# Optimization experiments

Measured on AMD Instinct MI355X. Metric: run time of the kernel, lower is better.

The kernel has to match this reference:

```python
import jax, jax.numpy as jnp
import numpy as np

# static sizes (see shape_source)
OBJ_N, WALL_N, FLOOR_N = 192, 16, 1
T = OBJ_N + WALL_N + FLOOR_N          # 209 total nodes
R = T * T - T                          # 43472 directed edges (no self loops)
D = 512
STEPS = 4                              # feat_update_step (1 group)
OBJ_IN, WALL_IN, FLOOR_IN, REL_IN = 42, 15, 16, 2

# buildMap: all-pairs meshgrid edges, self-loops removed, one-hot subj/obj maps
_nd = ~np.eye(T, dtype=bool)
_si, _oi = np.meshgrid(np.arange(T), np.arange(T), indexing='ij')
_subj_idx = _si[_nd]
_obj_idx = _oi[_nd]
SUBJ_MAP = jnp.asarray((np.arange(T)[:, None] == _subj_idx[None, :]).astype(np.float32))  # [T,R]
OBJ_MAP = jnp.asarray((np.arange(T)[:, None] == _obj_idx[None, :]).astype(np.float32))    # [T,R]
TOTAL_MAP = jnp.ones((T, T), jnp.float32)
REL_IDX = jnp.asarray(np.nonzero(_nd.reshape(-1))[0])  # [R] static gather indices


def setup_inputs():
    key = jax.random.key(0)
    ks = iter(jax.random.split(key, 64))
    def w(shape):
        return jax.random.normal(next(ks), shape, jnp.float32) * 0.01  # normal_(0, 0.01)
    inp = {
        'cat_object_feature': jax.random.normal(next(ks), (1, OBJ_N, OBJ_IN), jnp.float32),
        'cat_wall_feature': jax.random.normal(next(ks), (1, WALL_N, WALL_IN), jnp.float32),
        'cat_floor_feature': jax.random.normal(next(ks), (1, FLOOR_N, FLOOR_IN), jnp.float32),
        'cat_relation_feature': jax.random.normal(next(ks), (1, OBJ_N * OBJ_N, REL_IN), jnp.float32),
    }
    for name, din in [('obj', OBJ_IN), ('wall', WALL_IN), ('floor', FLOOR_IN), ('rel', REL_IN)]:
        inp[name + '_w1'] = w((din, D)); inp[name + '_b1'] = jnp.zeros((D,), jnp.float32)
        inp[name + '_w2'] = w((D, D));   inp[name + '_b2'] = jnp.zeros((D,), jnp.float32)
    inp['collect_w'] = w((5, D, D))                       # 5 _Collection_Unit fc weights
    inp['collect_b'] = jnp.zeros((5, D), jnp.float32)
    for name in ['tr', 'eu', 'sc']:
        inp[name + '_w1'] = w((D, D // 2)); inp[name + '_b1'] = jnp.zeros((D // 2,), jnp.float32)
        inp[name + '_w2'] = w((D // 2, 3)); inp[name + '_b2'] = jnp.zeros((3,), jnp.float32)
    return inp


def _mlp(x, w1, b1, w2, b2):
    return jax.nn.relu(x @ w1 + b1) @ w2 + b2


def _head(x, w1, b1, w2, b2):
    # Linear -> LeakyReLU(0.2) -> Dropout(eval: identity) -> Linear
    return jax.nn.leaky_relu(x @ w1 + b1, 0.2) @ w2 + b2


def _collect(src, attn, w, b):
    # _Collection_Unit: attn @ relu(fc(src)) / (row_sum + 1e-7)
    fc = jax.nn.relu(src @ w + b)
    return (attn @ fc) / (attn.sum(1, keepdims=True) + 1e-7)


def reference(cat_object_feature, cat_wall_feature, cat_floor_feature, cat_relation_feature,
              obj_w1, obj_b1, obj_w2, obj_b2, wall_w1, wall_b1, wall_w2, wall_b2,
              floor_w1, floor_b1, floor_w2, floor_b2, rel_w1, rel_b1, rel_w2, rel_b2,
              collect_w, collect_b, tr_w1, tr_b1, tr_w2, tr_b2,
              eu_w1, eu_b1, eu_w2, eu_b2, sc_w1, sc_b1, sc_w2, sc_b2):
    tot = jnp.concatenate([
        _mlp(cat_object_feature[0], obj_w1, obj_b1, obj_w2, obj_b2),
        _mlp(cat_wall_feature[0], wall_w1, wall_b1, wall_w2, wall_b2),
        _mlp(cat_floor_feature[0], floor_w1, floor_b1, floor_w2, floor_b2)], axis=0)  # [T,D]
    emb_rel = _mlp(cat_relation_feature[0], rel_w1, rel_b1, rel_w2, rel_b2)
    padded = jnp.pad(emb_rel.reshape(OBJ_N, OBJ_N, D),
                     ((0, T - OBJ_N), (0, T - OBJ_N), (0, 0)), constant_values=0.001)
    rel = padded.reshape(T * T, D)[REL_IDX]  # mask_total_relation_feature [R,D]

    for _ in range(STEPS):
        s_obj = _collect(tot, TOTAL_MAP, collect_w[4], collect_b[4])
        s_rs = _collect(rel, SUBJ_MAP, collect_w[0], collect_b[0])
        s_ro = _collect(rel, OBJ_MAP, collect_w[1], collect_b[1])
        new_tot = tot + (s_obj + s_rs + s_ro) / 3.0          # _Update_Unit: target + source
        s_os = _collect(tot, SUBJ_MAP.T, collect_w[2], collect_b[2])
        s_oo = _collect(tot, OBJ_MAP.T, collect_w[3], collect_b[3])
        rel = rel + (s_os + s_oo) / 2.0
        tot = new_tot

    obj = tot[:OBJ_N]  # object_mask select
    return jnp.concatenate([
        _head(obj, tr_w1, tr_b1, tr_w2, tr_b2),
        _head(obj, eu_w1, eu_b1, eu_w2, eu_b2),
        _head(obj, sc_w1, sc_b1, sc_w2, sc_b2)], axis=-1)  # [OBJ_N, 9]
```

## Files before the change

### kernel.cpp

```cpp
#include <hip/hip_runtime.h>
#include <stdint.h>

typedef unsigned short u16;
typedef __attribute__((ext_vector_type(4))) float f32x4;
typedef __attribute__((ext_vector_type(8))) short s16x8;
typedef __attribute__((ext_vector_type(4))) short s16x4;

#define DD (512*512)

__device__ inline u16 f2bf(float f) {
  uint32_t u = __float_as_uint(f);
  u = (u + 0x7FFFu + ((u >> 16) & 1u)) >> 16;
  return (u16)u;
}
__device__ inline float bflo(uint32_t w) { return __uint_as_float(w << 16); }
__device__ inline float bfhi(uint32_t w) { return __uint_as_float(w & 0xFFFF0000u); }
__device__ inline f32x4 relu4(f32x4 v) {
  f32x4 r;
  r.x = fmaxf(v.x, 0.f); r.y = fmaxf(v.y, 0.f);
  r.z = fmaxf(v.z, 0.f); r.w = fmaxf(v.w, 0.f);
  return r;
}
__device__ inline f32x4 bf4(const u16* p) {
  uint2 w = *(const uint2*)p;
  f32x4 r; r.x = bflo(w.x); r.y = bfhi(w.x); r.z = bflo(w.y); r.w = bfhi(w.y);
  return r;
}
__device__ inline s16x4 pack4(f32x4 v) {
  s16x4 o;
  o[0] = (short)f2bf(v.x); o[1] = (short)f2bf(v.y);
  o[2] = (short)f2bf(v.z); o[3] = (short)f2bf(v.w);
  return o;
}
__device__ inline void gload16(const void* g, void* l) {
  __builtin_amdgcn_global_load_lds(
      (const __attribute__((address_space(1))) void*)g,
      (__attribute__((address_space(3))) void*)l, 16, 0, 0);
}

struct PrepP {
  const float *xo, *xw, *xf;
  const float *ow1, *ob1, *ww1, *wb1, *fw1, *fb1;
  float* hid;
  const float* rw2; u16* rw2b;
  const float* cw; u16* cwT;
  const float* cb; const float* rb2;
  float *b0b, *b0p, *b1b, *b1p;
  const float *xr, *rw1, *rb1; u16* Hh;
};

__global__ __launch_bounds__(256) void kprep(PrepP pp) {
  __shared__ __align__(16) float plds[1088];
  const int bid = blockIdx.x;
  const int t = threadIdx.x;
  if (bid < 209) {
    int tc = bid;
    const float* x; const float* w; const float* b; int K;
    if (tc < 192)      { x = pp.xo + tc * 42;         w = pp.ow1; b = pp.ob1; K = 42; }
    else if (tc < 208) { x = pp.xw + (tc - 192) * 15; w = pp.ww1; b = pp.wb1; K = 15; }
    else               { x = pp.xf;                   w = pp.fw1; b = pp.fb1; K = 16; }
    float* xs = plds;
    if (t < K) xs[t] = x[t];
    __syncthreads();
    #pragma unroll
    for (int dd = 0; dd < 2; dd++) {
      int d = t + dd * 256;
      float acc = b[d];
      for (int k = 0; k < K; k++) acc = fmaf(xs[k], w[k * 512 + d], acc);
      pp.hid[(size_t)tc * 512 + d] = fmaxf(acc, 0.f);
    }
  } else if (bid < 337) {
    int g = (bid - 209) * 256 + t;
    f32x4 a = *(const f32x4*)&pp.rw2[(size_t)g * 8];
    f32x4 b = *(const f32x4*)&pp.rw2[(size_t)g * 8 + 4];
    s16x8 o;
    o[0] = (short)f2bf(a.x); o[1] = (short)f2bf(a.y); o[2] = (short)f2bf(a.z); o[3] = (short)f2bf(a.w);
    o[4] = (short)f2bf(b.x); o[5] = (short)f2bf(b.y); o[6] = (short)f2bf(b.z); o[7] = (short)f2bf(b.w);
    *(s16x8*)&pp.rw2b[(size_t)g * 8] = o;
  } else if (bid < 1617) {
    int local = bid - 337;
    int bx = local & 15, by = (local >> 4) & 15, bz = local >> 8;
    float (*tile)[33] = (float(*)[33])plds;
    const float* src = pp.cw + (size_t)bz * DD;
    int k0 = bx * 32, n0 = by * 32;
    #pragma unroll
    for (int i = 0; i < 4; i++) {
      int idx = t + i * 256; int r = idx >> 5, c = idx & 31;
      tile[r][c] = src[(size_t)(k0 + r) * 512 + n0 + c];
    }
    __syncthreads();
    #pragma unroll
    for (int i = 0; i < 4; i++) {
      int idx = t + i * 256; int r = idx >> 5, c = idx & 31;
      pp.cwT[((size_t)bz * 512 + n0 + r) * 512 + k0 + c] = f2bf(tile[c][r]);
    }
  } else if (bid < 1625) {
    int bx = bid - 1617;
    int dl = t & 63;
    int d = bx * 64 + dl;
    int kg = t >> 6;
    const float* W0 = pp.cw;
    const float* W1 = pp.cw + DD;
    float a0 = 0, p0 = 0, a1 = 0, p1 = 0;
    for (int k = kg * 128; k < (kg + 1) * 128; ++k) {
      float w0 = W0[(size_t)k * 512 + d], w1 = W1[(size_t)k * 512 + d], r = pp.rb2[k];
      a0 = fmaf(r, w0, a0); p0 += w0;
      a1 = fmaf(r, w1, a1); p1 += w1;
    }
    float (*red)[4][64] = (float(*)[4][64])plds;
    red[0][kg][dl] = a0; red[1][kg][dl] = p0; red[2][kg][dl] = a1; red[3][kg][dl] = p1;
    __syncthreads();
    if (kg == 0) {
      float s0  = red[0][0][dl] + red[0][1][dl] + red[0][2][dl] + red[0][3][dl];
      float sp0 = red[1][0][dl] + red[1][1][dl] + red[1][2][dl] + red[1][3][dl];
      float s1  = red[2][0][dl] + red[2][1][dl] + red[2][2][dl] + red[2][3][dl];
      float sp1 = red[3][0][dl] + red[3][1][dl] + red[3][2][dl] + red[3][3][dl];
      float bb0 = pp.cb[0 * 512 + d], bb1 = pp.cb[1 * 512 + d];
      pp.b0b[d] = s0 + bb0;
      pp.b0p[d] = 0.001f * sp0 + bb0;
      pp.b1b[d] = s1 + bb1;
      pp.b1p[d] = 0.001f * sp1 + bb1;
    }
  } else {
    int gid = (bid - 1625) * 256 + t;
    int m = gid >> 6;
    int dg = (gid & 63) * 8;
    float x0 = pp.xr[m * 2], x1 = pp.xr[m * 2 + 1];
    s16x8 o;
    #pragma unroll
    for (int j = 0; j < 8; j++) {
      int dd = dg + j;
      float v = fmaf(x0, pp.rw1[dd], fmaf(x1, pp.rw1[512 + dd], pp.rb1[dd]));
      o[j] = (short)f2bf(fmaxf(v, 0.f));
    }
    *(s16x8*)&pp.Hh[(size_t)m * 512 + dg] = o;
  }
}

struct SJob { const float* A; const float* B; const float* bias; float* C; u16* Cb; int M; int act; };
struct SJobs { SJob j[4]; int cum[5]; int njobs; };
struct PMJob { const u16* A; const u16* BT; float* C; };
struct MidP { SJobs sj; PMJob mj[2]; };

__global__ __launch_bounds__(256) void kmid(MidP mp) {
  __shared__ __align__(16) u16 mlds[24576];
  const int t = threadIdx.x;
  if (blockIdx.x < 64) {
    int bi = blockIdx.x;
    int ji = 0;
    while (ji + 1 < mp.sj.njobs && bi >= mp.sj.cum[ji + 1]) ji++;
    SJob job = mp.sj.j[ji];
    int local = bi - mp.sj.cum[ji];
    int mt = local >> 3, nt = local & 7;
    int m0 = mt * 32, n0 = nt * 64;
    float* As = (float*)mlds;
    float* Bs = As + 32 * 36;
    int row = t >> 3;
    int cg  = (t & 7) * 8;
    f32x4 accA = {0.f,0.f,0.f,0.f}, accB = {0.f,0.f,0.f,0.f};
    for (int k0 = 0; k0 < 512; k0 += 32) {
      __syncthreads();
      {
        int ar = t >> 3, ac = (t & 7) * 4;
        f32x4 av = {0.f,0.f,0.f,0.f};
        if (m0 + ar < job.M) av = *(const f32x4*)&job.A[(size_t)(m0 + ar) * 512 + k0 + ac];
        *(f32x4*)&As[ar * 36 + ac] = av;
      }
      #pragma unroll
      for (int i = 0; i < 2; i++) {
        int idx = t + i * 256;
        int bk = idx >> 4, bn = (idx & 15) * 4;
        *(f32x4*)&Bs[bk * 64 + bn] = *(const f32x4*)&job.B[(size_t)(k0 + bk) * 512 + n0 + bn];
      }
      __syncthreads();
      #pragma unroll
      for (int kk = 0; kk < 32; kk += 4) {
        f32x4 a4 = *(const f32x4*)&As[row * 36 + kk];
        #pragma unroll
        for (int q = 0; q < 4; q++) {
          f32x4 b0 = *(const f32x4*)&Bs[(kk + q) * 64 + cg];
          f32x4 b1 = *(const f32x4*)&Bs[(kk + q) * 64 + cg + 4];
          float av = a4[q];
          accA += av * b0;
          accB += av * b1;
        }
      }
    }
    int r = m0 + row;
    if (r < job.M) {
      f32x4 b0 = {0.f,0.f,0.f,0.f}, b1 = {0.f,0.f,0.f,0.f};
      if (job.bias) { b0 = *(const f32x4*)&job.bias[n0 + cg]; b1 = *(const f32x4*)&job.bias[n0 + cg + 4]; }
      f32x4 o0 = accA + b0, o1 = accB + b1;
      if (job.act) { o0 = relu4(o0); o1 = relu4(o1); }
      *(f32x4*)&job.C[(size_t)r * 512 + n0 + cg]     = o0;
      *(f32x4*)&job.C[(size_t)r * 512 + n0 + cg + 4] = o1;
      if (job.Cb) {
        s16x8 ob;
        ob[0] = (short)f2bf(o0.x); ob[1] = (short)f2bf(o0.y);
        ob[2] = (short)f2bf(o0.z); ob[3] = (short)f2bf(o0.w);
        ob[4] = (short)f2bf(o1.x); ob[5] = (short)f2bf(o1.y);
        ob[6] = (short)f2bf(o1.z); ob[7] = (short)f2bf(o1.w);
        *(s16x8*)&job.Cb[(size_t)r * 512 + n0 + cg] = ob;
      }
    }
  } else {
    int bi = blockIdx.x - 64;
    int ji = bi >> 5;
    int local = bi & 31;
    PMJob job = mp.mj[ji];
    int m0 = (local >> 2) * 64, n0 = (local & 3) * 128;
    u16* smem = mlds;
    const int lane = t & 63;
    const int wave = t >> 6;
    const int wm = wave >> 1, wn = wave & 1;
    const int r16 = lane & 15;
    const int kq = lane >> 4;
    f32x4 acc[2][4];
    #pragma unroll
    for (int i = 0; i < 2; i++)
      #pragma unroll
      for (int j = 0; j < 4; j++) acc[i][j] = (f32x4){0.f,0.f,0.f,0.f};
    const u16* gA[2]; int laofs[2];
    const u16* gB[4]; int lbofs[4];
    #pragma unroll
    for (int i = 0; i < 2; i++) {
      int seg = i * 256 + t;
      int row = seg >> 3, s = seg & 7;
      gA[i] = job.A + (size_t)(m0 + row) * 512 + ((s ^ (row & 7)) << 3);
      laofs[i] = (i * 256 + (t & 192)) << 3;
    }
    #pragma unroll
    for (int i = 0; i < 4; i++) {
      int seg = i * 256 + t;
      int row = seg >> 3, s = seg & 7;
      gB[i] = job.BT + (size_t)(n0 + row) * 512 + ((s ^ (row & 7)) << 3);
      lbofs[i] = 4096 + ((i * 256 + (t & 192)) << 3);
    }
    #pragma unroll
    for (int i = 0; i < 2; i++) gload16(gA[i], smem + laofs[i]);
    #pragma unroll
    for (int i = 0; i < 4; i++) gload16(gB[i], smem + lbofs[i]);
    __syncthreads();
    int buf = 0;
    for (int it = 0; it < 8; ++it) {
      if (it < 7) {
        int nb = (buf ^ 1) * 12288;
        int k0n = (it + 1) * 64;
        #pragma unroll
        for (int i = 0; i < 2; i++) gload16(gA[i] + k0n, smem + nb + laofs[i]);
        #pragma unroll
        for (int i = 0; i < 4; i++) gload16(gB[i] + k0n, smem + nb + lbofs[i]);
      }
      const u16* Ab = smem + buf * 12288;
      const u16* Bb = Ab + 4096;
      #pragma unroll
      for (int kh = 0; kh < 2; kh++) {
        s16x8 af[2], bfr[4];
        #pragma unroll
        for (int i = 0; i < 2; i++) {
          int r = wm * 32 + i * 16 + r16;
          af[i] = *(const s16x8*)&Ab[r * 64 + (((kq + kh * 4) ^ (r & 7)) << 3)];
        }
        #pragma unroll
        for (int j = 0; j < 4; j++) {
          int r = wn * 64 + j * 16 + r16;
          bfr[j] = *(const s16x8*)&Bb[r * 64 + (((kq + kh * 4) ^ (r & 7)) << 3)];
        }
        #pragma unroll
        for (int i = 0; i < 2; i++)
          #pragma unroll
          for (int j = 0; j < 4; j++)
            acc[i][j] = __builtin_amdgcn_mfma_f32_16x16x32_bf16(af[i], bfr[j], acc[i][j], 0, 0, 0);
      }
      __syncthreads();
      buf ^= 1;
    }
    #pragma unroll
    for (int i = 0; i < 2; i++) {
      int rbase = m0 + wm * 32 + i * 16 + (lane >> 4) * 4;
      #pragma unroll
      for (int r = 0; r < 4; r++) {
        int grow = rbase + r;
        #pragma unroll
        for (int j = 0; j < 4; j++)
          job.C[(size_t)grow * 512 + n0 + wn * 64 + j * 16 + r16] = acc[i][j][r];
      }
    }
  }
}

__global__ __launch_bounds__(256) void kwct(const float* __restrict__ tmp0, const float* __restrict__ tmp1,
                                            u16* __restrict__ WcT) {
  __shared__ float tile[32][33];
  const float* src = blockIdx.z ? tmp1 : tmp0;
  int k0 = blockIdx.x * 32, n0 = blockIdx.y * 32;
  int t = threadIdx.x;
  #pragma unroll
  for (int i = 0; i < 4; i++) {
    int idx = t + i * 256; int r = idx >> 5, c = idx & 31;
    tile[r][c] = src[(size_t)(k0 + r) * 512 + n0 + c];
  }
  __syncthreads();
  #pragma unroll
  for (int i = 0; i < 4; i++) {
    int idx = t + i * 256; int r = idx >> 5, c = idx & 31;
    WcT[((size_t)blockIdx.z * 512 + n0 + r) * 512 + k0 + c] = f2bf(tile[c][r]);
  }
}

__global__ __launch_bounds__(256) void kbig(const u16* __restrict__ Hh, const u16* __restrict__ WcT,
                                            u16* __restrict__ Q0, u16* __restrict__ Q1T) {
  __shared__ u16 smem[2 * 16384];
  const int bid = blockIdx.x;
  const int xcd = bid & 7;
  const int lp = bid >> 3;
  const int m0 = (xcd * 36 + (lp >> 3)) * 128;
  const int n0 = (lp & 7) * 128;
  const int t = threadIdx.x;
  const int lane = t & 63;
  const int wave = t >> 6;
  const int wm = wave >> 1, wn = wave & 1;
  const int r16 = lane & 15;
  const int kq = lane >> 4;
  f32x4 acc[4][4];
  #pragma unroll
  for (int i = 0; i < 4; i++)
    #pragma unroll
    for (int j = 0; j < 4; j++) acc[i][j] = (f32x4){0.f, 0.f, 0.f, 0.f};

  const u16* gA[4]; const u16* gB[4];
  int lofs[4];
  #pragma unroll
  for (int i = 0; i < 4; i++) {
    int seg = i * 256 + t;
    int row = seg >> 3, s = seg & 7;
    int sw = (s ^ (row & 7)) << 3;
    gA[i] = Hh  + (size_t)(m0 + row) * 512 + sw;
    gB[i] = WcT + (size_t)(n0 + row) * 512 + sw;
    lofs[i] = (i * 256 + (t & 192)) << 3;
  }
  #pragma unroll
  for (int i = 0; i < 4; i++) {
    gload16(gA[i], smem + lofs[i]);
    gload16(gB[i], smem + 8192 + lofs[i]);
  }
  __syncthreads();
  int buf = 0;
  for (int it = 0; it < 8; ++it) {
    if (it < 7) {
      int nb = (buf ^ 1) * 16384;
      int k0n = (it + 1) * 64;
      #pragma unroll
      for (int i = 0; i < 4; i++) {
        gload16(gA[i] + k0n, smem + nb + lofs[i]);
        gload16(gB[i] + k0n, smem + nb + 8192 + lofs[i]);
      }
    }
    const u16* Ab = smem + buf * 16384;
    const u16* Bb = Ab + 8192;
    #pragma unroll
    for (int kh = 0; kh < 2; kh++) {
      s16x8 af[4], bfr[4];
      #pragma unroll
      for (int i = 0; i < 4; i++) {
        int r = wm * 64 + i * 16 + r16;
        af[i] = *(const s16x8*)&Ab[r * 64 + (((kq + kh * 4) ^ (r & 7)) << 3)];
      }
      #pragma unroll
      for (int j = 0; j < 4; j++) {
        int r = wn * 64 + j * 16 + r16;
        bfr[j] = *(const s16x8*)&Bb[r * 64 + (((kq + kh * 4) ^ (r & 7)) << 3)];
      }
      #pragma unroll
      for (int i = 0; i < 4; i++)
        #pragma unroll
        for (int j = 0; j < 4; j++)
          acc[i][j] = __builtin_amdgcn_mfma_f32_16x16x32_bf16(af[i], bfr[j], acc[i][j], 0, 0, 0);
    }
    __syncthreads();
    buf ^= 1;
  }

  float* Cs = (float*)smem;
  const bool isQ1 = (n0 >= 512);
  #pragma unroll
  for (int c = 0; c < 4; c++) {
    __syncthreads();
    if ((c >> 1) == wm) {
      const int cbase = (c & 1) * 32;
      #pragma unroll
      for (int ii = 0; ii < 2; ii++) {
        const int i = (cbase >> 4) + ii;
        #pragma unroll
        for (int j = 0; j < 4; j++) {
          #pragma unroll
          for (int r = 0; r < 4; r++) {
            int rrow = i * 16 + (lane >> 4) * 4 + r - cbase;
            int ccol = wn * 64 + j * 16 + r16;
            Cs[rrow * 132 + ccol] = acc[i][j][r];
          }
        }
      }
    }
    __syncthreads();
    const int row = t >> 3, cg = (t & 7) * 16;
    const int gm = m0 + c * 32 + row;
    s16x8 o0, o1;
    #pragma unroll
    for (int x = 0; x < 8; x++) o0[x] = (short)f2bf(Cs[row * 132 + cg + x]);
    #pragma unroll
    for (int x = 0; x < 8; x++) o1[x] = (short)f2bf(Cs[row * 132 + cg + 8 + x]);
    u16* dst;
    if (!isQ1) {
      dst = Q0 + (size_t)gm * 512 + (n0 + cg);
    } else {
      int s = gm / 192, o = gm - s * 192;
      dst = Q1T + ((size_t)o * 192 + s) * 512 + (n0 - 512 + cg);
    }
    *(s16x8*)dst = o0;
    *(s16x8*)(dst + 8) = o1;
  }
}

struct MJob { const u16* A; const u16* BT; const float* bias; float* C; int Mreal; int act; };
struct MJobs { MJob j[8]; int cum[9]; int njobs; };

__global__ __launch_bounds__(256) void kmg(MJobs js) {
  int bi = blockIdx.x;
  int ji = 0;
  while (ji + 1 < js.njobs && bi >= js.cum[ji + 1]) ji++;
  MJob job = js.j[ji];
  int local = bi - js.cum[ji];
  int m0 = (local >> 2) * 64, n0 = (local & 3) * 128;

  __shared__ u16 smem[2 * 12288];
  const int t = threadIdx.x;
  const int lane = t & 63;
  const int wave = t >> 6;
  const int wm = wave >> 1, wn = wave & 1;
  const int r16 = lane & 15;
  const int kq = lane >> 4;
  f32x4 acc[2][4];
  #pragma unroll
  for (int i = 0; i < 2; i++)
    #pragma unroll
    for (int j = 0; j < 4; j++) acc[i][j] = (f32x4){0.f,0.f,0.f,0.f};

  const u16* gA[2]; int laofs[2];
  const u16* gB[4]; int lbofs[4];
  #pragma unroll
  for (int i = 0; i < 2; i++) {
    int seg = i * 256 + t;
    int row = seg >> 3, s = seg & 7;
    gA[i] = job.A + (size_t)(m0 + row) * 512 + ((s ^ (row & 7)) << 3);
    laofs[i] = (i * 256 + (t & 192)) << 3;
  }
  #pragma unroll
  for (int i = 0; i < 4; i++) {
    int seg = i * 256 + t;
    int row = seg >> 3, s = seg & 7;
    gB[i] = job.BT + (size_t)(n0 + row) * 512 + ((s ^ (row & 7)) << 3);
    lbofs[i] = 4096 + ((i * 256 + (t & 192)) << 3);
  }

  #pragma unroll
  for (int i = 0; i < 2; i++) gload16(gA[i], smem + laofs[i]);
  #pragma unroll
  for (int i = 0; i < 4; i++) gload16(gB[i], smem + lbofs[i]);
  __syncthreads();

  int buf = 0;
  for (int it = 0; it < 8; ++it) {
    if (it < 7) {
      int nb = (buf ^ 1) * 12288;
      int k0n = (it + 1) * 64;
      #pragma unroll
      for (int i = 0; i < 2; i++) gload16(gA[i] + k0n, smem + nb + laofs[i]);
      #pragma unroll
      for (int i = 0; i < 4; i++) gload16(gB[i] + k0n, smem + nb + lbofs[i]);
    }
    const u16* Ab = smem + buf * 12288;
    const u16* Bb = Ab + 4096;
    #pragma unroll
    for (int kh = 0; kh < 2; kh++) {
      s16x8 af[2], bfr[4];
      #pragma unroll
      for (int i = 0; i < 2; i++) {
        int r = wm * 32 + i * 16 + r16;
        af[i] = *(const s16x8*)&Ab[r * 64 + (((kq + kh * 4) ^ (r & 7)) << 3)];
      }
      #pragma unroll
      for (int j = 0; j < 4; j++) {
        int r = wn * 64 + j * 16 + r16;
        bfr[j] = *(const s16x8*)&Bb[r * 64 + (((kq + kh * 4) ^ (r & 7)) << 3)];
      }
      #pragma unroll
      for (int i = 0; i < 2; i++)
        #pragma unroll
        for (int j = 0; j < 4; j++)
          acc[i][j] = __builtin_amdgcn_mfma_f32_16x16x32_bf16(af[i], bfr[j], acc[i][j], 0, 0, 0);
    }
    __syncthreads();
    buf ^= 1;
  }

  float bj[4] = {0.f, 0.f, 0.f, 0.f};
  if (job.bias) {
    #pragma unroll
    for (int j = 0; j < 4; j++) bj[j] = job.bias[n0 + wn * 64 + j * 16 + r16];
  }
  #pragma unroll
  for (int i = 0; i < 2; i++) {
    int rbase = m0 + wm * 32 + i * 16 + (lane >> 4) * 4;
    #pragma unroll
    for (int r = 0; r < 4; r++) {
      int grow = rbase + r;
      if (grow < job.Mreal) {
        #pragma unroll
        for (int j = 0; j < 4; j++) {
          float v = acc[i][j][r] + bj[j];
          if (job.act) v = fmaxf(v, 0.f);
          job.C[(size_t)grow * 512 + n0 + wn * 64 + j * 16 + r16] = v;
        }
      }
    }
  }
}

__global__ __launch_bounds__(128) void kpass(const u16* __restrict__ Q0, const u16* __restrict__ Q1T,
                                             const float* __restrict__ u0, const float* __restrict__ v0,
                                             const float* __restrict__ u1, const float* __restrict__ v1,
                                             const float* __restrict__ b0b, const float* __restrict__ b1b,
                                             const float* __restrict__ fc4,
                                             float* __restrict__ part, float* __restrict__ sobj) {
  int z = blockIdx.z;
  int t = threadIdx.x;
  if (z == 2) {
    if (blockIdx.y != 0 || blockIdx.x >= 4) return;
    int d = blockIdx.x * 128 + t;
    float s = 0.f;
    for (int r = 0; r < 209; ++r) s += fc4[(size_t)r * 512 + d];
    sobj[d] = s;
    return;
  }
  int so = blockIdx.x;
  if (so >= 192) return;
  int chunk = blockIdx.y;
  int d = t * 4;
  const u16* Q = z ? Q1T : Q0;
  const float* fixtab  = z ? v1 : u0;
  const float* looptab = z ? u1 : v0;
  const float* bb = z ? b1b : b0b;
  f32x4 fix = *(const f32x4*)&fixtab[(size_t)so * 512 + d] + *(const f32x4*)&bb[d];
  f32x4 acc = {0.f,0.f,0.f,0.f};
  const u16* qbase = Q + ((size_t)so * 192 + chunk * 48) * 512 + d;
  const float* lbase = looptab + (size_t)(chunk * 48) * 512 + d;
  #pragma unroll 4
  for (int r = 0; r < 48; ++r) {
    f32x4 qa = bf4(qbase + (size_t)r * 512);
    f32x4 vv = *(const f32x4*)(lbase + (size_t)r * 512);
    f32x4 val = qa + fix + vv;
    acc.x += fmaxf(val.x, 0.f); acc.y += fmaxf(val.y, 0.f);
    acc.z += fmaxf(val.z, 0.f); acc.w += fmaxf(val.w, 0.f);
  }
  *(f32x4*)&part[(((size_t)z * 209 + so) * 4 + chunk) * 512 + d] = acc;
}

__global__ __launch_bounds__(128) void kfinish(const u16* __restrict__ Q0, const u16* __restrict__ Q1T,
                                               const float* __restrict__ u0, const float* __restrict__ v0,
                                               const float* __restrict__ u1, const float* __restrict__ v1,
                                               const float* __restrict__ b0b, const float* __restrict__ b0p,
                                               const float* __restrict__ b1b, const float* __restrict__ b1p,
                                               const float* __restrict__ part, const float* __restrict__ sobj,
                                               const float* __restrict__ fcS, const float* __restrict__ fcO,
                                               float* __restrict__ tot, float* __restrict__ addS,
                                               float* __restrict__ addO,
                                               u16* __restrict__ totb, u16* __restrict__ aSb,
                                               u16* __restrict__ aOb) {
  int tt = blockIdx.x;
  int t = threadIdx.x;
  int d = t * 4;
  size_t rowoff = (size_t)tt * 512 + d;
  f32x4 u0r = *(const f32x4*)&u0[rowoff];
  f32x4 v0r = *(const f32x4*)&v0[rowoff];
  f32x4 u1r = *(const f32x4*)&u1[rowoff];
  f32x4 v1r = *(const f32x4*)&v1[rowoff];
  f32x4 B0B = *(const f32x4*)&b0b[d];
  f32x4 B0P = *(const f32x4*)&b0p[d];
  f32x4 B1B = *(const f32x4*)&b1b[d];
  f32x4 B1P = *(const f32x4*)&b1p[d];
  f32x4 srs = {0.f,0.f,0.f,0.f}, sro = {0.f,0.f,0.f,0.f};
  if (tt < 192) {
    #pragma unroll
    for (int c = 0; c < 4; c++) {
      srs += *(const f32x4*)&part[(((size_t)0 * 209 + tt) * 4 + c) * 512 + d];
      sro += *(const f32x4*)&part[(((size_t)1 * 209 + tt) * 4 + c) * 512 + d];
    }
    for (int o = 192; o < 209; o++) srs += relu4(B0P + u0r + *(const f32x4*)&v0[(size_t)o * 512 + d]);
    for (int s = 192; s < 209; s++) sro += relu4(B1P + *(const f32x4*)&u1[(size_t)s * 512 + d] + v1r);
    f32x4 qd0 = bf4(Q0 + ((size_t)tt * 193) * 512 + d);
    srs -= relu4(qd0 + u0r + v0r + B0B);
    f32x4 qd1 = bf4(Q1T + ((size_t)tt * 193) * 512 + d);
    sro -= relu4(qd1 + u1r + v1r + B1B);
  } else {
    for (int o = 0; o < 209; o++) srs += relu4(B0P + u0r + *(const f32x4*)&v0[(size_t)o * 512 + d]);
    srs -= relu4(B0P + u0r + v0r);
    for (int s = 0; s < 209; s++) sro += relu4(B1P + *(const f32x4*)&u1[(size_t)s * 512 + d] + v1r);
    sro -= relu4(B1P + u1r + v1r);
  }
  const float inv209 = 1.0f / (float)(209.0 + 1e-7);
  const float inv208 = 1.0f / (float)(208.0 + 1e-7);
  const float invrel = 0.5f / (float)(1.0 + 1e-7);
  f32x4 so4 = *(const f32x4*)&sobj[d] * inv209;
  srs *= inv208;
  sro *= inv208;
  f32x4 tt4 = *(const f32x4*)&tot[rowoff];
  tt4 += (so4 + srs + sro) * (1.0f / 3.0f);
  *(f32x4*)&tot[rowoff] = tt4;
  f32x4 aS = *(const f32x4*)&addS[rowoff] + *(const f32x4*)&fcS[rowoff] * invrel;
  f32x4 aO = *(const f32x4*)&addO[rowoff] + *(const f32x4*)&fcO[rowoff] * invrel;
  *(f32x4*)&addS[rowoff] = aS;
  *(f32x4*)&addO[rowoff] = aO;
  *(s16x4*)&totb[rowoff] = pack4(tt4);
  *(s16x4*)&aSb[rowoff]  = pack4(aS);
  *(s16x4*)&aOb[rowoff]  = pack4(aO);
}

__global__ __launch_bounds__(256) void kheads(const float* __restrict__ tot,
    const float* __restrict__ w1a, const float* __restrict__ b1a, const float* __restrict__ w2a, const float* __restrict__ b2a,
    const float* __restrict__ w1b, const float* __restrict__ b1bb, const float* __restrict__ w2b, const float* __restrict__ b2b,
    const float* __restrict__ w1c, const float* __restrict__ b1c, const float* __restrict__ w2c, const float* __restrict__ b2c,
    float* __restrict__ out) {
  int row = blockIdx.x;
  int t = threadIdx.x;
  __shared__ float xs[512];
  xs[t] = tot[(size_t)row * 512 + t];
  xs[t + 256] = tot[(size_t)row * 512 + 256 + t];
  __syncthreads();
  const float* W1[3] = {w1a, w1b, w1c};
  const float* B1[3] = {b1a, b1bb, b1c};
  const float* W2[3] = {w2a, w2b, w2c};
  float p[9];
  #pragma unroll
  for (int hd = 0; hd < 3; hd++) {
    float a = B1[hd][t];
    for (int k = 0; k < 512; k += 4) {
      f32x4 x4 = *(const f32x4*)&xs[k];
      a = fmaf(x4.x, W1[hd][(size_t)(k + 0) * 256 + t], a);
      a = fmaf(x4.y, W1[hd][(size_t)(k + 1) * 256 + t], a);
      a = fmaf(x4.z, W1[hd][(size_t)(k + 2) * 256 + t], a);
      a = fmaf(x4.w, W1[hd][(size_t)(k + 3) * 256 + t], a);
    }
    float h = a > 0.f ? a : 0.2f * a;
    p[hd * 3 + 0] = h * W2[hd][t * 3 + 0];
    p[hd * 3 + 1] = h * W2[hd][t * 3 + 1];
    p[hd * 3 + 2] = h * W2[hd][t * 3 + 2];
  }
  __shared__ float red[9][256];
  #pragma unroll
  for (int c = 0; c < 9; c++) red[c][t] = p[c];
  __syncthreads();
  for (int s = 128; s > 0; s >>= 1) {
    if (t < s) {
      #pragma unroll
      for (int c = 0; c < 9; c++) red[c][t] += red[c][t + s];
    }
    __syncthreads();
  }
  if (t < 9) {
    const float* B2[3] = {b2a, b2b, b2c};
    out[(size_t)row * 9 + t] = red[t][0] + B2[t / 3][t % 3];
  }
}

extern "C" void kernel_launch(void* const* d_in, const int* in_sizes, int n_in,
                              void* d_out, int out_size, void* d_ws, size_t ws_size,
                              hipStream_t stream) {
  const float* xo  = (const float*)d_in[0];
  const float* xw  = (const float*)d_in[1];
  const float* xf  = (const float*)d_in[2];
  const float* xr  = (const float*)d_in[3];
  const float* ow1 = (const float*)d_in[4];
  const float* ob1 = (const float*)d_in[5];
  const float* ow2 = (const float*)d_in[6];
  const float* ob2 = (const float*)d_in[7];
  const float* ww1 = (const float*)d_in[8];
  const float* wb1 = (const float*)d_in[9];
  const float* ww2 = (const float*)d_in[10];
  const float* wb2 = (const float*)d_in[11];
  const float* fw1 = (const float*)d_in[12];
  const float* fb1 = (const float*)d_in[13];
  const float* fw2 = (const float*)d_in[14];
  const float* fb2 = (const float*)d_in[15];
  const float* rw1 = (const float*)d_in[16];
  const float* rb1 = (const float*)d_in[17];
  const float* rw2 = (const float*)d_in[18];
  const float* rb2 = (const float*)d_in[19];
  const float* cw  = (const float*)d_in[20];
  const float* cb  = (const float*)d_in[21];
  const float* tw1 = (const float*)d_in[22];
  const float* tb1 = (const float*)d_in[23];
  const float* tw2 = (const float*)d_in[24];
  const float* tb2 = (const float*)d_in[25];
  const float* ew1 = (const float*)d_in[26];
  const float* eb1 = (const float*)d_in[27];
  const float* ew2 = (const float*)d_in[28];
  const float* eb2 = (const float*)d_in[29];
  const float* sw1 = (const float*)d_in[30];
  const float* sb1 = (const float*)d_in[31];
  const float* sw2 = (const float*)d_in[32];
  const float* sb2 = (const float*)d_in[33];
  float* out = (float*)d_out;

  char* p = (char*)d_ws;
  auto alloc = [&](size_t bytes) { char* r = p; p += (bytes + 255) & ~(size_t)255; return r; };
  const size_t SZ = 209 * 512 * sizeof(float);
  const size_t BSZ = 256 * 512 * sizeof(u16);
  float* tot  = (float*)alloc(SZ);
  float* addS = (float*)alloc(SZ);
  float* addO = (float*)alloc(SZ);
  u16*   totb = (u16*)alloc(BSZ);
  u16*   aSb  = (u16*)alloc(BSZ);
  u16*   aOb  = (u16*)alloc(BSZ);
  float* fc4  = (float*)alloc(SZ);
  float* fcS  = (float*)alloc(SZ);
  float* fcO  = (float*)alloc(SZ);
  float* u0   = (float*)alloc(SZ);
  float* v0   = (float*)alloc(SZ);
  float* u1   = (float*)alloc(SZ);
  float* v1   = (float*)alloc(SZ);
  float* hid  = (float*)alloc(SZ);
  float* sobj = (float*)alloc(512 * sizeof(float));
  float* part = (float*)alloc((size_t)2 * 209 * 4 * 512 * sizeof(float));
  float* b0b  = (float*)alloc(512 * sizeof(float));
  float* b0p  = (float*)alloc(512 * sizeof(float));
  float* b1b  = (float*)alloc(512 * sizeof(float));
  float* b1p  = (float*)alloc(512 * sizeof(float));
  float* tmp0 = (float*)alloc((size_t)DD * sizeof(float));
  float* tmp1 = (float*)alloc((size_t)DD * sizeof(float));
  u16* rw2b = (u16*)alloc((size_t)DD * sizeof(u16));
  u16* cwT  = (u16*)alloc((size_t)5 * DD * sizeof(u16));
  u16* Hh  = (u16*)alloc((size_t)36864 * 512 * sizeof(u16));
  u16* WcT = (u16*)alloc((size_t)1024 * 512 * sizeof(u16));
  u16* Q0  = (u16*)alloc((size_t)36864 * 512 * sizeof(u16));
  u16* Q1T = (u16*)alloc((size_t)36864 * 512 * sizeof(u16));

  hipMemsetAsync(addS, 0, 2 * SZ + 3 * BSZ, stream);

  PrepP pp;
  pp.xo = xo; pp.xw = xw; pp.xf = xf;
  pp.ow1 = ow1; pp.ob1 = ob1; pp.ww1 = ww1; pp.wb1 = wb1; pp.fw1 = fw1; pp.fb1 = fb1;
  pp.hid = hid;
  pp.rw2 = rw2; pp.rw2b = rw2b;
  pp.cw = cw; pp.cwT = cwT;
  pp.cb = cb; pp.rb2 = rb2;
  pp.b0b = b0b; pp.b0p = b0p; pp.b1b = b1b; pp.b1p = b1p;
  pp.xr = xr; pp.rw1 = rw1; pp.rb1 = rb1; pp.Hh = Hh;
  kprep<<<10841, 256, 0, stream>>>(pp);

  MidP mp{};
  mp.sj.j[0] = { hid,             ow2, ob2, tot,             totb,             192, 0 };
  mp.sj.j[1] = { hid + 192 * 512, ww2, wb2, tot + 192 * 512, totb + 192 * 512,  16, 0 };
  mp.sj.j[2] = { hid + 208 * 512, fw2, fb2, tot + 208 * 512, totb + 208 * 512,   1, 0 };
  mp.sj.njobs = 3;
  mp.sj.cum[0] = 0;
  for (int i = 0; i < 3; i++) mp.sj.cum[i + 1] = mp.sj.cum[i] + ((mp.sj.j[i].M + 31) / 32) * 8;
  mp.mj[0] = { rw2b, cwT,      tmp0 };
  mp.mj[1] = { rw2b, cwT + DD, tmp1 };
  kmid<<<128, 256, 0, stream>>>(mp);

  kwct<<<dim3(16, 16, 2), 256, 0, stream>>>(tmp0, tmp1, WcT);
  kbig<<<2304, 256, 0, stream>>>(Hh, WcT, Q0, Q1T);

  MJobs st{};
  st.j[0] = { totb, cwT + 4 * DD, cb + 4 * 512, fc4, 209, 1 };
  st.j[1] = { totb, cwT + 2 * DD, cb + 2 * 512, fcS, 209, 1 };
  st.j[2] = { totb, cwT + 3 * DD, cb + 3 * 512, fcO, 209, 1 };
  st.j[3] = { aSb,  cwT,          nullptr,      u0,  209, 0 };
  st.j[4] = { aOb,  cwT,          nullptr,      v0,  209, 0 };
  st.j[5] = { aSb,  cwT + DD,     nullptr,      u1,  209, 0 };
  st.j[6] = { aOb,  cwT + DD,     nullptr,      v1,  209, 0 };
  st.njobs = 7;
  st.cum[0] = 0;
  for (int i = 0; i < 7; i++) st.cum[i + 1] = st.cum[i] + 4 * 4;

  for (int step = 0; step < 4; step++) {
    kmg<<<st.cum[7], 256, 0, stream>>>(st);
    kpass<<<dim3(209, 4, 3), 128, 0, stream>>>(Q0, Q1T, u0, v0, u1, v1, b0b, b1b, fc4, part, sobj);
    kfinish<<<209, 128, 0, stream>>>(Q0, Q1T, u0, v0, u1, v1, b0b, b0p, b1b, b1p,
                                     part, sobj, fcS, fcO, tot, addS, addO, totb, aSb, aOb);
  }

  kheads<<<192, 256, 0, stream>>>(tot, tw1, tb1, tw2, tb2, ew1, eb1, ew2, eb2, sw1, sb1, sw2, sb2, out);
}
```

Baseline: 414.0 us.

## Fuse pass/finish via atomic counters, fold transpose into kmid, retile kmg

```diff
diff --git a/kernel.cpp b/kernel.cpp
--- a/kernel.cpp
+++ b/kernel.cpp
@@ -139,7 +139,7 @@
 
 struct SJob { const float* A; const float* B; const float* bias; float* C; u16* Cb; int M; int act; };
 struct SJobs { SJob j[4]; int cum[5]; int njobs; };
-struct PMJob { const u16* A; const u16* BT; float* C; };
+struct PMJob { const u16* A; const u16* BT; u16* W; };
 struct MidP { SJobs sj; PMJob mj[2]; };
 
 __global__ __launch_bounds__(256) void kmid(MidP mp) {
@@ -277,34 +277,16 @@
     }
     #pragma unroll
     for (int i = 0; i < 2; i++) {
-      int rbase = m0 + wm * 32 + i * 16 + (lane >> 4) * 4;
-      #pragma unroll
-      for (int r = 0; r < 4; r++) {
-        int grow = rbase + r;
+      int rbase = m0 + wm * 32 + i * 16 + kq * 4;
+      #pragma unroll
+      for (int j = 0; j < 4; j++) {
+        int col = n0 + wn * 64 + j * 16 + r16;
+        s16x4 o;
         #pragma unroll
-        for (int j = 0; j < 4; j++)
-          job.C[(size_t)grow * 512 + n0 + wn * 64 + j * 16 + r16] = acc[i][j][r];
-      }
-    }
-  }
-}
-
-__global__ __launch_bounds__(256) void kwct(const float* __restrict__ tmp0, const float* __restrict__ tmp1,
-                                            u16* __restrict__ WcT) {
-  __shared__ float tile[32][33];
-  const float* src = blockIdx.z ? tmp1 : tmp0;
-  int k0 = blockIdx.x * 32, n0 = blockIdx.y * 32;
-  int t = threadIdx.x;
-  #pragma unroll
-  for (int i = 0; i < 4; i++) {
-    int idx = t + i * 256; int r = idx >> 5, c = idx & 31;
-    tile[r][c] = src[(size_t)(k0 + r) * 512 + n0 + c];
-  }
-  __syncthreads();
-  #pragma unroll
-  for (int i = 0; i < 4; i++) {
-    int idx = t + i * 256; int r = idx >> 5, c = idx & 31;
-    WcT[((size_t)blockIdx.z * 512 + n0 + r) * 512 + k0 + c] = f2bf(tile[c][r]);
+        for (int r = 0; r < 4; r++) o[r] = (short)f2bf(acc[i][j][r]);
+        *(s16x4*)&job.W[(size_t)col * 512 + rbase] = o;
+      }
+    }
   }
 }
 
@@ -422,7 +404,7 @@
   }
 }
 
-struct MJob { const u16* A; const u16* BT; const float* bias; float* C; int Mreal; int act; };
+struct MJob { const u16* A; const u16* BT; const float* bias; float* C; float* csum; int Mreal; int mode; };
 struct MJobs { MJob j[8]; int cum[9]; int njobs; };
 
 __global__ __launch_bounds__(256) void kmg(MJobs js) {
@@ -431,199 +413,223 @@
   while (ji + 1 < js.njobs && bi >= js.cum[ji + 1]) ji++;
   MJob job = js.j[ji];
   int local = bi - js.cum[ji];
-  int m0 = (local >> 2) * 64, n0 = (local & 3) * 128;
-
-  __shared__ u16 smem[2 * 12288];
+  int m0 = (local >> 3) * 64, n0 = (local & 7) * 64;
+
+  __shared__ u16 smem[2 * 16384];
   const int t = threadIdx.x;
   const int lane = t & 63;
-  const int wave = t >> 6;
-  const int wm = wave >> 1, wn = wave & 1;
+  const int wv = t >> 6;
   const int r16 = lane & 15;
   const int kq = lane >> 4;
-  f32x4 acc[2][4];
-  #pragma unroll
-  for (int i = 0; i < 2; i++)
-    #pragma unroll
-    for (int j = 0; j < 4; j++) acc[i][j] = (f32x4){0.f,0.f,0.f,0.f};
-
-  const u16* gA[2]; int laofs[2];
-  const u16* gB[4]; int lbofs[4];
-  #pragma unroll
-  for (int i = 0; i < 2; i++) {
-    int seg = i * 256 + t;
-    int row = seg >> 3, s = seg & 7;
-    gA[i] = job.A + (size_t)(m0 + row) * 512 + ((s ^ (row & 7)) << 3);
-    laofs[i] = (i * 256 + (t & 192)) << 3;
-  }
+  f32x4 acc[4];
+  #pragma unroll
+  for (int j = 0; j < 4; j++) acc[j] = (f32x4){0.f,0.f,0.f,0.f};
+
+  const u16* gA[4]; const u16* gB[4]; int lofs[4];
   #pragma unroll
   for (int i = 0; i < 4; i++) {
     int seg = i * 256 + t;
-    int row = seg >> 3, s = seg & 7;
-    gB[i] = job.BT + (size_t)(n0 + row) * 512 + ((s ^ (row & 7)) << 3);
-    lbofs[i] = 4096 + ((i * 256 + (t & 192)) << 3);
-  }
-
-  #pragma unroll
-  for (int i = 0; i < 2; i++) gload16(gA[i], smem + laofs[i]);
-  #pragma unroll
-  for (int i = 0; i < 4; i++) gload16(gB[i], smem + lbofs[i]);
+    int row = seg >> 4, s = seg & 15;
+    int sw = (s ^ (row & 15)) << 3;
+    gA[i] = job.A  + (size_t)(m0 + row) * 512 + sw;
+    gB[i] = job.BT + (size_t)(n0 + row) * 512 + sw;
+    lofs[i] = (i * 256 + (t & 192)) << 3;
+  }
+  #pragma unroll
+  for (int i = 0; i < 4; i++) {
+    gload16(gA[i], smem + lofs[i]);
+    gload16(gB[i], smem + 8192 + lofs[i]);
+  }
   __syncthreads();
-
   int buf = 0;
-  for (int it = 0; it < 8; ++it) {
-    if (it < 7) {
-      int nb = (buf ^ 1) * 12288;
-      int k0n = (it + 1) * 64;
-      #pragma unroll
-      for (int i = 0; i < 2; i++) gload16(gA[i] + k0n, smem + nb + laofs[i]);
-      #pragma unroll
-      for (int i = 0; i < 4; i++) gload16(gB[i] + k0n, smem + nb + lbofs[i]);
-    }
-    const u16* Ab = smem + buf * 12288;
-    const u16* Bb = Ab + 4096;
-    #pragma unroll
-    for (int kh = 0; kh < 2; kh++) {
-      s16x8 af[2], bfr[4];
-      #pragma unroll
-      for (int i = 0; i < 2; i++) {
-        int r = wm * 32 + i * 16 + r16;
-        af[i] = *(const s16x8*)&Ab[r * 64 + (((kq + kh * 4) ^ (r & 7)) << 3)];
-      }
+  for (int it = 0; it < 4; ++it) {
+    if (it < 3) {
+      int nb = (buf ^ 1) * 16384;
+      int k0n = (it + 1) * 128;
+      #pragma unroll
+      for (int i = 0; i < 4; i++) {
+        gload16(gA[i] + k0n, smem + nb + lofs[i]);
+        gload16(gB[i] + k0n, smem + nb + 8192 + lofs[i]);
+      }
+    }
+    const u16* Ab = smem + buf * 16384;
+    const u16* Bb = Ab + 8192;
+    #pragma unroll
+    for (int kh = 0; kh < 4; kh++) {
+      int q = kh * 4 + kq;
+      int ra = wv * 16 + r16;
+      s16x8 af = *(const s16x8*)&Ab[ra * 128 + ((q ^ (ra & 15)) << 3)];
       #pragma unroll
       for (int j = 0; j < 4; j++) {
-        int r = wn * 64 + j * 16 + r16;
-        bfr[j] = *(const s16x8*)&Bb[r * 64 + (((kq + kh * 4) ^ (r & 7)) << 3)];
-      }
-      #pragma unroll
-      for (int i = 0; i < 2; i++)
-        #pragma unroll
-        for (int j = 0; j < 4; j++)
-          acc[i][j] = __builtin_amdgcn_mfma_f32_16x16x32_bf16(af[i], bfr[j], acc[i][j], 0, 0, 0);
+        int rb = j * 16 + r16;
+        s16x8 bfr = *(const s16x8*)&Bb[rb * 128 + ((q ^ (rb & 15)) << 3)];
+        acc[j] = __builtin_amdgcn_mfma_f32_16x16x32_bf16(af, bfr, acc[j], 0, 0, 0);
+      }
     }
     __syncthreads();
     buf ^= 1;
   }
 
-  float bj[4] = {0.f, 0.f, 0.f, 0.f};
-  if (job.bias) {
-    #pragma unroll
-    for (int j = 0; j < 4; j++) bj[j] = job.bias[n0 + wn * 64 + j * 16 + r16];
-  }
-  #pragma unroll
-  for (int i = 0; i < 2; i++) {
-    int rbase = m0 + wm * 32 + i * 16 + (lane >> 4) * 4;
+  float bj[4] = {0.f,0.f,0.f,0.f};
+  if (job.mode) {
+    #pragma unroll
+    for (int j = 0; j < 4; j++) bj[j] = job.bias[n0 + j * 16 + r16];
+  }
+  if (job.mode == 2) {
+    float fsum[4];
+    #pragma unroll
+    for (int j = 0; j < 4; j++) {
+      fsum[j] = 0.f;
+      #pragma unroll
+      for (int r = 0; r < 4; r++) {
+        int grow = m0 + wv * 16 + kq * 4 + r;
+        if (grow < job.Mreal) fsum[j] += fmaxf(acc[j][r] + bj[j], 0.f);
+      }
+    }
+    float (*red)[64] = (float(*)[64])smem;
+    int cix = wv * 4 + kq;
+    #pragma unroll
+    for (int j = 0; j < 4; j++) red[cix][j * 16 + r16] = fsum[j];
+    __syncthreads();
+    if (t < 64) {
+      float s = 0.f;
+      #pragma unroll
+      for (int c = 0; c < 16; c++) s += red[c][t];
+      job.csum[(size_t)(m0 >> 6) * 512 + n0 + t] = s;
+    }
+    return;
+  }
+  #pragma unroll
+  for (int j = 0; j < 4; j++) {
+    int col = n0 + j * 16 + r16;
     #pragma unroll
     for (int r = 0; r < 4; r++) {
-      int grow = rbase + r;
+      int grow = m0 + wv * 16 + kq * 4 + r;
       if (grow < job.Mreal) {
-        #pragma unroll
-        for (int j = 0; j < 4; j++) {
-          float v = acc[i][j][r] + bj[j];
-          if (job.act) v = fmaxf(v, 0.f);
-          job.C[(size_t)grow * 512 + n0 + wn * 64 + j * 16 + r16] = v;
-        }
-      }
-    }
-  }
-}
-
-__global__ __launch_bounds__(128) void kpass(const u16* __restrict__ Q0, const u16* __restrict__ Q1T,
-                                             const float* __restrict__ u0, const float* __restrict__ v0,
-                                             const float* __restrict__ u1, const float* __restrict__ v1,
-                                             const float* __restrict__ b0b, const float* __restrict__ b1b,
-                                             const float* __restrict__ fc4,
-                                             float* __restrict__ part, float* __restrict__ sobj) {
-  int z = blockIdx.z;
-  int t = threadIdx.x;
-  if (z == 2) {
-    if (blockIdx.y != 0 || blockIdx.x >= 4) return;
-    int d = blockIdx.x * 128 + t;
-    float s = 0.f;
-    for (int r = 0; r < 209; ++r) s += fc4[(size_t)r * 512 + d];
-    sobj[d] = s;
+        float v = acc[j][r] + bj[j];
+        if (job.mode == 1) v = fmaxf(v, 0.f);
+        job.C[(size_t)grow * 512 + col] = v;
+      }
+    }
+  }
+}
+
+struct PFP {
+  const u16 *Q0, *Q1T;
+  const float *u0, *v0, *u1, *v1;
+  const float *b0b, *b0p, *b1b, *b1p;
+  const float *fc4part;
+  const float *fcS, *fcO;
+  float *part, *sobj;
+  float *tot, *addS, *addO;
+  u16 *totb, *aSb, *aOb;
+  int *cnt;
+  int *sflag;
+};
+
+__global__ __launch_bounds__(128) void kpassfin(PFP P) {
+  const int bid = blockIdx.x;
+  const int t = threadIdx.x;
+  __shared__ int isLast;
+
+  if (bid < 4) {
+    int d = bid * 128 + t;
+    P.sobj[d] = P.fc4part[d] + P.fc4part[512 + d] + P.fc4part[1024 + d] + P.fc4part[1536 + d];
+    __threadfence();
+    __syncthreads();
+    if (t == 0) __hip_atomic_fetch_add(P.sflag, 1, __ATOMIC_ACQ_REL, __HIP_MEMORY_SCOPE_AGENT);
     return;
   }
-  int so = blockIdx.x;
-  if (so >= 192) return;
-  int chunk = blockIdx.y;
-  int d = t * 4;
-  const u16* Q = z ? Q1T : Q0;
-  const float* fixtab  = z ? v1 : u0;
-  const float* looptab = z ? u1 : v0;
-  const float* bb = z ? b1b : b0b;
-  f32x4 fix = *(const f32x4*)&fixtab[(size_t)so * 512 + d] + *(const f32x4*)&bb[d];
-  f32x4 acc = {0.f,0.f,0.f,0.f};
-  const u16* qbase = Q + ((size_t)so * 192 + chunk * 48) * 512 + d;
-  const float* lbase = looptab + (size_t)(chunk * 48) * 512 + d;
-  #pragma unroll 4
-  for (int r = 0; r < 48; ++r) {
-    f32x4 qa = bf4(qbase + (size_t)r * 512);
-    f32x4 vv = *(const f32x4*)(lbase + (size_t)r * 512);
-    f32x4 val = qa + fix + vv;
-    acc.x += fmaxf(val.x, 0.f); acc.y += fmaxf(val.y, 0.f);
-    acc.z += fmaxf(val.z, 0.f); acc.w += fmaxf(val.w, 0.f);
-  }
-  *(f32x4*)&part[(((size_t)z * 209 + so) * 4 + chunk) * 512 + d] = acc;
-}
-
-__global__ __launch_bounds__(128) void kfinish(const u16* __restrict__ Q0, const u16* __restrict__ Q1T,
-                                               const float* __restrict__ u0, const float* __restrict__ v0,
-                                               const float* __restrict__ u1, const float* __restrict__ v1,
-                                               const float* __restrict__ b0b, const float* __restrict__ b0p,
-                                               const float* __restrict__ b1b, const float* __restrict__ b1p,
-                                               const float* __restrict__ part, const float* __restrict__ sobj,
-                                               const float* __restrict__ fcS, const float* __restrict__ fcO,
-                                               float* __restrict__ tot, float* __restrict__ addS,
-                                               float* __restrict__ addO,
-                                               u16* __restrict__ totb, u16* __restrict__ aSb,
-                                               u16* __restrict__ aOb) {
-  int tt = blockIdx.x;
-  int t = threadIdx.x;
+
+  int tt;
+  if (bid < 21) {
+    tt = bid + 188;
+  } else {
+    int j = bid - 21;
+    int so = j >> 3;
+    int z = (j >> 2) & 1;
+    int chunk = j & 3;
+    int d = t * 4;
+    const u16* Q = z ? P.Q1T : P.Q0;
+    const float* fixtab  = z ? P.v1 : P.u0;
+    const float* looptab = z ? P.u1 : P.v0;
+    const float* bb = z ? P.b1b : P.b0b;
+    f32x4 fix = *(const f32x4*)&fixtab[(size_t)so * 512 + d] + *(const f32x4*)&bb[d];
+    f32x4 acc = {0.f,0.f,0.f,0.f};
+    const u16* qbase = Q + ((size_t)so * 192 + chunk * 48) * 512 + d;
+    const float* lbase = looptab + (size_t)(chunk * 48) * 512 + d;
+    #pragma unroll 4
+    for (int r = 0; r < 48; ++r) {
+      f32x4 qa = bf4(qbase + (size_t)r * 512);
+      f32x4 vv = *(const f32x4*)(lbase + (size_t)r * 512);
+      f32x4 val = qa + fix + vv;
+      acc.x += fmaxf(val.x, 0.f); acc.y += fmaxf(val.y, 0.f);
+      acc.z += fmaxf(val.z, 0.f); acc.w += fmaxf(val.w, 0.f);
+    }
+    *(f32x4*)&P.part[(((size_t)z * 209 + so) * 4 + chunk) * 512 + d] = acc;
+    __threadfence();
+    __syncthreads();
+    if (t == 0) {
+      int old = __hip_atomic_fetch_add(&P.cnt[so], 1, __ATOMIC_ACQ_REL, __HIP_MEMORY_SCOPE_AGENT);
+      isLast = (old == 7);
+    }
+    __syncthreads();
+    if (!isLast) return;
+    tt = so;
+  }
+
+  if (t == 0) {
+    while (__hip_atomic_load(P.sflag, __ATOMIC_ACQUIRE, __HIP_MEMORY_SCOPE_AGENT) < 4)
+      __builtin_amdgcn_s_sleep(2);
+  }
+  __syncthreads();
+  __threadfence();
+
   int d = t * 4;
   size_t rowoff = (size_t)tt * 512 + d;
-  f32x4 u0r = *(const f32x4*)&u0[rowoff];
-  f32x4 v0r = *(const f32x4*)&v0[rowoff];
-  f32x4 u1r = *(const f32x4*)&u1[rowoff];
-  f32x4 v1r = *(const f32x4*)&v1[rowoff];
-  f32x4 B0B = *(const f32x4*)&b0b[d];
-  f32x4 B0P = *(const f32x4*)&b0p[d];
-  f32x4 B1B = *(const f32x4*)&b1b[d];
-  f32x4 B1P = *(const f32x4*)&b1p[d];
+  f32x4 u0r = *(const f32x4*)&P.u0[rowoff];
+  f32x4 v0r = *(const f32x4*)&P.v0[rowoff];
+  f32x4 u1r = *(const f32x4*)&P.u1[rowoff];
+  f32x4 v1r = *(const f32x4*)&P.v1[rowoff];
+  f32x4 B0B = *(const f32x4*)&P.b0b[d];
+  f32x4 B0P = *(const f32x4*)&P.b0p[d];
+  f32x4 B1B = *(const f32x4*)&P.b1b[d];
+  f32x4 B1P = *(const f32x4*)&P.b1p[d];
   f32x4 srs = {0.f,0.f,0.f,0.f}, sro = {0.f,0.f,0.f,0.f};
   if (tt < 192) {
     #pragma unroll
     for (int c = 0; c < 4; c++) {
-      srs += *(const f32x4*)&part[(((size_t)0 * 209 + tt) * 4 + c) * 512 + d];
-      sro += *(const f32x4*)&part[(((size_t)1 * 209 + tt) * 4 + c) * 512 + d];
-    }
-    for (int o = 192; o < 209; o++) srs += relu4(B0P + u0r + *(const f32x4*)&v0[(size_t)o * 512 + d]);
-    for (int s = 192; s < 209; s++) sro += relu4(B1P + *(const f32x4*)&u1[(size_t)s * 512 + d] + v1r);
-    f32x4 qd0 = bf4(Q0 + ((size_t)tt * 193) * 512 + d);
+      srs += *(const f32x4*)&P.part[(((size_t)0 * 209 + tt) * 4 + c) * 512 + d];
+      sro += *(const f32x4*)&P.part[(((size_t)1 * 209 + tt) * 4 + c) * 512 + d];
+    }
+    for (int o = 192; o < 209; o++) srs += relu4(B0P + u0r + *(const f32x4*)&P.v0[(size_t)o * 512 + d]);
+    for (int s = 192; s < 209; s++) sro += relu4(B1P + *(const f32x4*)&P.u1[(size_t)s * 512 + d] + v1r);
+    f32x4 qd0 = bf4(P.Q0 + ((size_t)tt * 193) * 512 + d);
     srs -= relu4(qd0 + u0r + v0r + B0B);
-    f32x4 qd1 = bf4(Q1T + ((size_t)tt * 193) * 512 + d);
+    f32x4 qd1 = bf4(P.Q1T + ((size_t)tt * 193) * 512 + d);
     sro -= relu4(qd1 + u1r + v1r + B1B);
   } else {
-    for (int o = 0; o < 209; o++) srs += relu4(B0P + u0r + *(const f32x4*)&v0[(size_t)o * 512 + d]);
+    for (int o = 0; o < 209; o++) srs += relu4(B0P + u0r + *(const f32x4*)&P.v0[(size_t)o * 512 + d]);
     srs -= relu4(B0P + u0r + v0r);
-    for (int s = 0; s < 209; s++) sro += relu4(B1P + *(const f32x4*)&u1[(size_t)s * 512 + d] + v1r);
+    for (int s = 0; s < 209; s++) sro += relu4(B1P + *(const f32x4*)&P.u1[(size_t)s * 512 + d] + v1r);
     sro -= relu4(B1P + u1r + v1r);
   }
   const float inv209 = 1.0f / (float)(209.0 + 1e-7);
   const float inv208 = 1.0f / (float)(208.0 + 1e-7);
   const float invrel = 0.5f / (float)(1.0 + 1e-7);
-  f32x4 so4 = *(const f32x4*)&sobj[d] * inv209;
+  f32x4 so4 = *(const f32x4*)&P.sobj[d] * inv209;
   srs *= inv208;
   sro *= inv208;
-  f32x4 tt4 = *(const f32x4*)&tot[rowoff];
+  f32x4 tt4 = *(const f32x4*)&P.tot[rowoff];
   tt4 += (so4 + srs + sro) * (1.0f / 3.0f);
-  *(f32x4*)&tot[rowoff] = tt4;
-  f32x4 aS = *(const f32x4*)&addS[rowoff] + *(const f32x4*)&fcS[rowoff] * invrel;
-  f32x4 aO = *(const f32x4*)&addO[rowoff] + *(const f32x4*)&fcO[rowoff] * invrel;
-  *(f32x4*)&addS[rowoff] = aS;
-  *(f32x4*)&addO[rowoff] = aO;
-  *(s16x4*)&totb[rowoff] = pack4(tt4);
-  *(s16x4*)&aSb[rowoff]  = pack4(aS);
-  *(s16x4*)&aOb[rowoff]  = pack4(aO);
+  *(f32x4*)&P.tot[rowoff] = tt4;
+  f32x4 aS = *(const f32x4*)&P.addS[rowoff] + *(const f32x4*)&P.fcS[rowoff] * invrel;
+  f32x4 aO = *(const f32x4*)&P.addO[rowoff] + *(const f32x4*)&P.fcO[rowoff] * invrel;
+  *(f32x4*)&P.addS[rowoff] = aS;
+  *(f32x4*)&P.addO[rowoff] = aO;
+  *(s16x4*)&P.totb[rowoff] = pack4(tt4);
+  *(s16x4*)&P.aSb[rowoff]  = pack4(aS);
+  *(s16x4*)&P.aOb[rowoff]  = pack4(aO);
 }
 
 __global__ __launch_bounds__(256) void kheads(const float* __restrict__ tot,
@@ -722,7 +728,8 @@
   u16*   totb = (u16*)alloc(BSZ);
   u16*   aSb  = (u16*)alloc(BSZ);
   u16*   aOb  = (u16*)alloc(BSZ);
-  float* fc4  = (float*)alloc(SZ);
+  int*   sync = (int*)alloc(4096);
+  float* fc4part = (float*)alloc(4 * 512 * sizeof(float));
   float* fcS  = (float*)alloc(SZ);
   float* fcO  = (float*)alloc(SZ);
   float* u0   = (float*)alloc(SZ);
@@ -736,8 +743,6 @@
   float* b0p  = (float*)alloc(512 * sizeof(float));
   float* b1b  = (float*)alloc(512 * sizeof(float));
   float* b1p  = (float*)alloc(512 * sizeof(float));
-  float* tmp0 = (float*)alloc((size_t)DD * sizeof(float));
-  float* tmp1 = (float*)alloc((size_t)DD * sizeof(float));
   u16* rw2b = (u16*)alloc((size_t)DD * sizeof(u16));
   u16* cwT  = (u16*)alloc((size_t)5 * DD * sizeof(u16));
   u16* Hh  = (u16*)alloc((size_t)36864 * 512 * sizeof(u16));
@@ -745,7 +750,7 @@
   u16* Q0  = (u16*)alloc((size_t)36864 * 512 * sizeof(u16));
   u16* Q1T = (u16*)alloc((size_t)36864 * 512 * sizeof(u16));
 
-  hipMemsetAsync(addS, 0, 2 * SZ + 3 * BSZ, stream);
+  hipMemsetAsync(addS, 0, 2 * SZ + 3 * BSZ + 4096, stream);
 
   PrepP pp;
   pp.xo = xo; pp.xw = xw; pp.xf = xf;
@@ -765,30 +770,38 @@
   mp.sj.njobs = 3;
   mp.sj.cum[0] = 0;
   for (int i = 0; i < 3; i++) mp.sj.cum[i + 1] = mp.sj.cum[i] + ((mp.sj.j[i].M + 31) / 32) * 8;
-  mp.mj[0] = { rw2b, cwT,      tmp0 };
-  mp.mj[1] = { rw2b, cwT + DD, tmp1 };
+  mp.mj[0] = { rw2b, cwT,      WcT };
+  mp.mj[1] = { rw2b, cwT + DD, WcT + DD };
   kmid<<<128, 256, 0, stream>>>(mp);
 
-  kwct<<<dim3(16, 16, 2), 256, 0, stream>>>(tmp0, tmp1, WcT);
   kbig<<<2304, 256, 0, stream>>>(Hh, WcT, Q0, Q1T);
 
   MJobs st{};
-  st.j[0] = { totb, cwT + 4 * DD, cb + 4 * 512, fc4, 209, 1 };
-  st.j[1] = { totb, cwT + 2 * DD, cb + 2 * 512, fcS, 209, 1 };
-  st.j[2] = { totb, cwT + 3 * DD, cb + 3 * 512, fcO, 209, 1 };
-  st.j[3] = { aSb,  cwT,          nullptr,      u0,  209, 0 };
-  st.j[4] = { aOb,  cwT,          nullptr,      v0,  209, 0 };
-  st.j[5] = { aSb,  cwT + DD,     nullptr,      u1,  209, 0 };
-  st.j[6] = { aOb,  cwT + DD,     nullptr,      v1,  209, 0 };
+  st.j[0] = { totb, cwT + 4 * DD, cb + 4 * 512, nullptr, fc4part, 209, 2 };
+  st.j[1] = { totb, cwT + 2 * DD, cb + 2 * 512, fcS, nullptr, 209, 1 };
+  st.j[2] = { totb, cwT + 3 * DD, cb + 3 * 512, fcO, nullptr, 209, 1 };
+  st.j[3] = { aSb,  cwT,          nullptr,      u0,  nullptr, 209, 0 };
+  st.j[4] = { aOb,  cwT,          nullptr,      v0,  nullptr, 209, 0 };
+  st.j[5] = { aSb,  cwT + DD,     nullptr,      u1,  nullptr, 209, 0 };
+  st.j[6] = { aOb,  cwT + DD,     nullptr,      v1,  nullptr, 209, 0 };
   st.njobs = 7;
   st.cum[0] = 0;
-  for (int i = 0; i < 7; i++) st.cum[i + 1] = st.cum[i] + 4 * 4;
+  for (int i = 0; i < 7; i++) st.cum[i + 1] = st.cum[i] + 4 * 8;
 
   for (int step = 0; step < 4; step++) {
     kmg<<<st.cum[7], 256, 0, stream>>>(st);
-    kpass<<<dim3(209, 4, 3), 128, 0, stream>>>(Q0, Q1T, u0, v0, u1, v1, b0b, b1b, fc4, part, sobj);
-    kfinish<<<209, 128, 0, stream>>>(Q0, Q1T, u0, v0, u1, v1, b0b, b0p, b1b, b1p,
-                                     part, sobj, fcS, fcO, tot, addS, addO, totb, aSb, aOb);
+    PFP pf;
+    pf.Q0 = Q0; pf.Q1T = Q1T;
+    pf.u0 = u0; pf.v0 = v0; pf.u1 = u1; pf.v1 = v1;
+    pf.b0b = b0b; pf.b0p = b0p; pf.b1b = b1b; pf.b1p = b1p;
+    pf.fc4part = fc4part;
+    pf.fcS = fcS; pf.fcO = fcO;
+    pf.part = part; pf.sobj = sobj;
+    pf.tot = tot; pf.addS = addS; pf.addO = addO;
+    pf.totb = totb; pf.aSb = aSb; pf.aOb = aOb;
+    pf.cnt = sync + step * 192;
+    pf.sflag = sync + 768 + step;
+    kpassfin<<<1557, 128, 0, stream>>>(pf);
   }
 
   kheads<<<192, 256, 0, stream>>>(tot, tw1, tb1, tw2, tb2, ew1, eb1, ew2, eb2, sw1, sb1, sw2, sb2, out);
```

Measured after the change: 835.3 us. +101.8%, slower.
